# Kernel optimization log

Hardware: AMD Instinct MI355X
Metric: run time of the kernel (lower is better)

Reference implementation:

```python
import jax, jax.numpy as jnp
import numpy as np

ORIENTATIONS = 9
CELL = (8, 8)
BLOCK = (3, 3)
EPS = 1e-5  # skimage L2 block-norm epsilon


def _hog_features(x):
    # transform_sqrt=True (gamma compression)
    img = jnp.sqrt(x)
    H, W = img.shape
    # skimage _hog_channel_gradient: central differences, zero at borders
    g_row = jnp.zeros_like(img).at[1:-1, :].set(img[2:, :] - img[:-2, :])
    g_col = jnp.zeros_like(img).at[:, 1:-1].set(img[:, 2:] - img[:, :-2])
    mag = jnp.hypot(g_row, g_col)
    # orientation in degrees, folded to [0, 180)
    ori = jnp.rad2deg(jnp.arctan2(g_row, g_col)) % 180.0

    cr, cc = CELL
    ncr, ncc = H // cr, W // cc
    mag_c = mag[: ncr * cr, : ncc * cc]
    ori_c = ori[: ncr * cr, : ncc * cc]
    unit = 180.0 / ORIENTATIONS

    # hard binning (skimage uses no interpolation); small fixed loop over bins
    hists = []
    for b in range(ORIENTATIONS):
        sel = (ori_c >= b * unit) & (ori_c < (b + 1) * unit)
        m = jnp.where(sel, mag_c, 0.0)
        # per-cell mean of selected magnitudes: [ncr, ncc]
        cell = m.reshape(ncr, cr, ncc, cc).mean(axis=(1, 3))
        hists.append(cell)
    hist = jnp.stack(hists, axis=-1)  # [ncr, ncc, orientations]

    br_n, bc_n = BLOCK
    nbr, nbc = ncr - br_n + 1, ncc - bc_n + 1
    # overlapping blocks: [nbr, nbc, br_n, bc_n, orientations]
    blocks = jnp.stack(
        [jnp.stack([hist[i : i + nbr, j : j + nbc] for j in range(bc_n)], axis=2)
         for i in range(br_n)],
        axis=2,
    )
    # L2 block normalization: b / sqrt(sum(b^2) + eps^2)
    denom = jnp.sqrt(jnp.sum(blocks * blocks, axis=(2, 3, 4), keepdims=True) + EPS ** 2)
    normalized = blocks / denom
    return normalized.reshape(-1)  # feature_vector=True


def setup_inputs() -> dict:
    key = jax.random.key(0)
    x = jax.random.uniform(key, (4096, 4096), dtype=jnp.float32)
    return {"x": x}


def reference(x):
    return _hog_features(x)
```

## Files before the change

kernel.cpp:

```cpp
#include <hip/hip_runtime.h>
#include <math.h>

#define H 4096
#define W 4096
#define NC 512
#define NB 510
#define ORI 9
#define NCELLS (NC * NC)
#define NOUT (NB * NB * 81)

__device__ __forceinline__ float fdlibm_atanf(float x) {
#pragma clang fp contract(off)
    const float one = 1.0f;
    const float aT0  = (float) 3.33333333333329318027e-01;
    const float aT1  = (float)-1.99999999998764832476e-01;
    const float aT2  = (float) 1.42857142725034663711e-01;
    const float aT3  = (float)-1.11111104054623557880e-01;
    const float aT4  = (float) 9.09088713343650656196e-02;
    const float aT5  = (float)-7.69187620504482999495e-02;
    const float aT6  = (float) 6.66107313738753120669e-02;
    const float aT7  = (float)-5.83357013379057348645e-02;
    const float aT8  = (float) 4.97687799461593236017e-02;
    const float aT9  = (float)-3.65315727442169155270e-02;
    const float aT10 = (float) 1.62858201153657823623e-02;
    const float athi[4] = {4.6364760399e-01f, 7.8539812565e-01f,
                           9.8279368877e-01f, 1.5707962513e+00f};
    const float atlo[4] = {5.0121582440e-09f, 3.7748947079e-08f,
                           3.4473217170e-08f, 7.5497894159e-08f};
    int hx = __float_as_int(x);
    int ix = hx & 0x7fffffff;
    int id;
    if (ix >= 0x4c800000) {
        if (ix > 0x7f800000) return x + x;
        float r = athi[3] + atlo[3];
        return (hx > 0) ? r : -r;
    }
    if (ix < 0x3ee00000) {
        if (ix < 0x31000000) return x;
        id = -1;
    } else {
        x = fabsf(x);
        if (ix < 0x3f980000) {
            if (ix < 0x3f300000) { id = 0; x = (2.0f * x - one) / (2.0f + x); }
            else                 { id = 1; x = (x - one) / (x + one); }
        } else {
            if (ix < 0x401c0000) { id = 2; x = (x - 1.5f) / (one + 1.5f * x); }
            else                 { id = 3; x = -1.0f / x; }
        }
    }
    float z = x * x;
    float w = z * z;
    float s1 = z * (aT0 + w * (aT2 + w * (aT4 + w * (aT6 + w * (aT8 + w * aT10)))));
    float s2 = w * (aT1 + w * (aT3 + w * (aT5 + w * (aT7 + w * aT9))));
    if (id < 0) return x - x * (s1 + s2);
    z = athi[id] - ((x * (s1 + s2) - atlo[id]) - x);
    return (hx < 0) ? -z : z;
}

__device__ __forceinline__ float fdlibm_atan2f(float y, float x) {
#pragma clang fp contract(off)
    const float tiny   = 1.0e-30f;
    const float pi     = 3.1415927410e+00f;
    const float pi_lo  = -8.7422776573e-08f;
    const float pi_o_2 = 1.5707963705e+00f;
    int hx = __float_as_int(x), ix = hx & 0x7fffffff;
    int hy = __float_as_int(y), iy = hy & 0x7fffffff;
    if (hx == 0x3f800000) return fdlibm_atanf(y);
    int m = ((hy >> 31) & 1) | ((hx >> 30) & 2);
    if (iy == 0) {
        switch (m) {
            case 0: case 1: return y;
            case 2: return pi + tiny;
            default: return -pi - tiny;
        }
    }
    if (ix == 0) return (hy < 0) ? -pi_o_2 - tiny : pi_o_2 + tiny;
    int k = (iy - ix) >> 23;
    float z;
    if (k > 26) { z = pi_o_2 + 0.5f * pi_lo; m &= 1; }
    else if (k < -26 && hx < 0) z = 0.0f;
    else z = fdlibm_atanf(fabsf(y / x));
    switch (m) {
        case 0: return z;
        case 1: return -z;
        case 2: return pi - (z - pi_lo);
        default: return (z - pi_lo) - pi;
    }
}

__device__ __forceinline__ int slow_bin_px(const float* __restrict__ x,
                                           int grow, int gc,
                                           bool row_ok, bool col_ok) {
#pragma clang fp contract(off)
    float gy = 0.0f, gx = 0.0f;
    if (row_ok)
        gy = sqrtf(x[(grow + 1) * W + gc]) - sqrtf(x[(grow - 1) * W + gc]);
    if (col_ok)
        gx = sqrtf(x[grow * W + gc + 1]) - sqrtf(x[grow * W + gc - 1]);
    float ang = fdlibm_atan2f(gy, gx);
    const float RAD2DEG = (float)(180.0 / 3.14159265358979323846264338328);
    float deg = ang * RAD2DEG;
    float m = fmodf(deg, 180.0f);
    if (m < 0.0f) m += 180.0f;
    int bin = (int)(m / 20.0f);
    if (bin < 9 && m >= (float)((bin + 1) * 20)) bin++;
    else if (bin > 0 && m < (float)(bin * 20)) bin--;
    return bin;
}

#define T20 ((float) 0.36397023426620236135)
#define T40 ((float) 0.83909963117728001176)
#define T60 ((float) 1.73205080756887729353)
#define T80 ((float) 5.67128181961771110517)

__global__ __launch_bounds__(256, 4) void hog_hist(const float* __restrict__ x,
                                                   float* __restrict__ hist,
                                                   float* __restrict__ q) {
    int t = threadIdx.x;
    int w = t >> 6, lane = t & 63;
    int wid = blockIdx.x * 4 + w;
    int crow = wid >> 6;
    int strip = wid & 63;
    int gc = (strip << 6) + lane;

    int r0 = (crow << 3) - 1;
    int rtop = (r0 < 0) ? 0 : r0;
    int rbot = (r0 + 9 > H - 1) ? (H - 1) : (r0 + 9);
    int gcl = (gc == 0) ? 0 : gc - 1;
    int gcr = (gc == W - 1) ? (W - 1) : gc + 1;

    float s[10], sl[8], sr[8];
    s[0] = x[rtop * W + gc];
#pragma unroll
    for (int k = 1; k < 9; ++k) s[k] = x[(r0 + k) * W + gc];
    s[9] = x[rbot * W + gc];
#pragma unroll
    for (int j = 0; j < 8; ++j) {
        int grow = (crow << 3) + j;
        sl[j] = x[grow * W + gcl];
        sr[j] = x[grow * W + gcr];
    }
#pragma unroll
    for (int k = 0; k < 10; ++k) s[k] = __builtin_amdgcn_sqrtf(s[k]);
#pragma unroll
    for (int j = 0; j < 8; ++j) {
        sl[j] = __builtin_amdgcn_sqrtf(sl[j]);
        sr[j] = __builtin_amdgcn_sqrtf(sr[j]);
    }

    bool col_ok = (gc >= 1) && (gc <= W - 2);
    float acc[9];
#pragma unroll
    for (int b = 0; b < 9; ++b) acc[b] = 0.0f;
    unsigned gbits = 0;

#pragma unroll
    for (int j = 0; j < 8; ++j) {
        int grow = (crow << 3) + j;
        bool row_ok = (grow >= 1) && (grow <= H - 2);
        float gy = row_ok ? (s[j + 2] - s[j]) : 0.0f;
        float gx = col_ok ? (sr[j] - sl[j]) : 0.0f;

        float a = fabsf(gy), b = fabsf(gx);
        float d1 = fmaf(b, -T20, a);
        float d2 = fmaf(b, -T40, a);
        float d3 = fmaf(b, -T60, a);
        float d4 = fmaf(b, -T80, a);
        int cnt = (d1 > 0.0f) + (d2 > 0.0f) + (d3 > 0.0f) + (d4 > 0.0f);
        bool opp = ((__float_as_int(gy) ^ __float_as_int(gx)) < 0);
        int bin = opp ? 8 - cnt : cnt;

        float cm = fminf(fminf(fabsf(d1), fabsf(d2)),
                         fminf(fminf(fabsf(d3), fabsf(d4)), a));
        bool guard = cm < fmaf(1e-5f, a + b, 4e-6f);
        if (guard) { gbits |= (1u << j); bin = 15; }

        float mag = __builtin_amdgcn_sqrtf(fmaf(gy, gy, gx * gx));
#pragma unroll
        for (int bb = 0; bb < 9; ++bb) acc[bb] += (bin == bb) ? mag : 0.0f;
    }

    if (__any(gbits != 0)) {
#pragma unroll
        for (int j = 0; j < 8; ++j) {
            if ((gbits >> j) & 1u) {
                int grow = (crow << 3) + j;
                bool row_ok = (grow >= 1) && (grow <= H - 2);
                int bin = slow_bin_px(x, grow, gc, row_ok, col_ok);
                float gy = row_ok ? (s[j + 2] - s[j]) : 0.0f;
                float gx = col_ok ? (sr[j] - sl[j]) : 0.0f;
                float mag = __builtin_amdgcn_sqrtf(fmaf(gy, gy, gx * gx));
#pragma unroll
                for (int bb = 0; bb < 9; ++bb) acc[bb] += (bin == bb) ? mag : 0.0f;
            }
        }
    }

#pragma unroll
    for (int st = 1; st <= 4; st <<= 1) {
#pragma unroll
        for (int b = 0; b < 9; ++b) acc[b] += __shfl_xor(acc[b], st, 64);
    }

    int cell = lane >> 3;
    int k = lane & 7;
    int cbase = crow * (NC * ORI) + strip * 72 + cell * 9;
    float hv = acc[0];
#pragma unroll
    for (int b = 1; b < 8; ++b) hv = (k == b) ? acc[b] : hv;
    hist[cbase + k] = hv * (1.0f / 64.0f);
    if (k == 0) {
        hist[cbase + 8] = acc[8] * (1.0f / 64.0f);
        float qq = 0.0f;
#pragma unroll
        for (int b = 0; b < 9; ++b) {
            float h = acc[b] * (1.0f / 64.0f);
            qq = fmaf(h, h, qq);
        }
        q[crow * NC + strip * 8 + cell] = qq;
    }
}

__global__ __launch_bounds__(256) void hog_inv(const float* __restrict__ q,
                                               float* __restrict__ inv) {
    int t = blockIdx.x * 256 + threadIdx.x;
    if (t >= NB * NB) return;
    int i = t / NB;
    int j = t - i * NB;
    float ssq = 0.0f;
#pragma unroll
    for (int bi = 0; bi < 3; ++bi)
#pragma unroll
        for (int bj = 0; bj < 3; ++bj)
            ssq += q[(i + bi) * NC + (j + bj)];
    inv[t] = 1.0f / sqrtf(ssq + 1e-10f);
}

__global__ __launch_bounds__(256) void hog_norm(const float* __restrict__ hist,
                                                const float* __restrict__ inv,
                                                float* __restrict__ out, int n) {
    int k = blockIdx.x * 256 + threadIdx.x;
    if (k >= n) return;
    int pidx = k / 81;
    int e = k - pidx * 81;
    int i = pidx / NB;
    int j = pidx - i * NB;
    int bi = e / 27;
    int r = e - bi * 27;
    int bj = r / 9;
    int o = r - bj * 9;
    out[k] = hist[((i + bi) * NC + (j + bj)) * ORI + o] * inv[pidx];
}

extern "C" void kernel_launch(void* const* d_in, const int* in_sizes, int n_in,
                              void* d_out, int out_size, void* d_ws, size_t ws_size,
                              hipStream_t stream) {
    const float* x = (const float*)d_in[0];
    float* out = (float*)d_out;
    float* hist = (float*)d_ws;
    float* inv  = hist + NCELLS * ORI;
    float* q = out + (NOUT - NCELLS);

    hog_hist<<<(NC * 64) / 4, 256, 0, stream>>>(x, hist, q);
    hog_inv<<<(NB * NB + 255) / 256, 256, 0, stream>>>(q, inv);
    hog_norm<<<(out_size + 255) / 256, 256, 0, stream>>>(hist, inv, out, out_size);
}
```

Measured before the change: 76.10 us.

## Use threshold-count accumulators, DPP reductions, and vectorized float4 normalization stores

The histogram kernel no longer does a per-pixel 9-way select-accumulate. It keeps ten running sums: threshold counts split by sign quadrant. The nine bins are recovered afterwards by differencing. The cross-lane shuffle reduction within 8-lane groups becomes DPP row operations, which avoids LDS-based shuffles. The normalization kernel writes four outputs per thread as float4 stores. The differencing can introduce small floating-point rounding differences compared with direct accumulation, and the float4 path assumes out_size is divisible by 4.

```diff
diff --git a/kernel.cpp b/kernel.cpp
--- a/kernel.cpp
+++ b/kernel.cpp
@@ -113,6 +113,16 @@
 #define T60 ((float) 1.73205080756887729353)
 #define T80 ((float) 5.67128181961771110517)
 
+__device__ __forceinline__ float dpp_add8(float v) {
+    int t = __builtin_amdgcn_update_dpp(0, __float_as_int(v), 0xB1, 0xF, 0xF, true);
+    v += __int_as_float(t);
+    t = __builtin_amdgcn_update_dpp(0, __float_as_int(v), 0x4E, 0xF, 0xF, true);
+    v += __int_as_float(t);
+    t = __builtin_amdgcn_update_dpp(0, __float_as_int(v), 0x141, 0xF, 0xF, true);
+    v += __int_as_float(t);
+    return v;
+}
+
 __global__ __launch_bounds__(256, 4) void hog_hist(const float* __restrict__ x,
                                                    float* __restrict__ hist,
                                                    float* __restrict__ q) {
@@ -149,9 +159,8 @@
     }
 
     bool col_ok = (gc >= 1) && (gc <= W - 2);
-    float acc[9];
-#pragma unroll
-    for (int b = 0; b < 9; ++b) acc[b] = 0.0f;
+    float SA = 0.f, TA1 = 0.f, TA2 = 0.f, TA3 = 0.f, TA4 = 0.f;
+    float SB = 0.f, TB1 = 0.f, TB2 = 0.f, TB3 = 0.f, TB4 = 0.f;
     unsigned gbits = 0;
 
 #pragma unroll
@@ -166,19 +175,33 @@
         float d2 = fmaf(b, -T40, a);
         float d3 = fmaf(b, -T60, a);
         float d4 = fmaf(b, -T80, a);
-        int cnt = (d1 > 0.0f) + (d2 > 0.0f) + (d3 > 0.0f) + (d4 > 0.0f);
-        bool opp = ((__float_as_int(gy) ^ __float_as_int(gx)) < 0);
-        int bin = opp ? 8 - cnt : cnt;
 
         float cm = fminf(fminf(fabsf(d1), fabsf(d2)),
                          fminf(fminf(fabsf(d3), fabsf(d4)), a));
         bool guard = cm < fmaf(1e-5f, a + b, 4e-6f);
-        if (guard) { gbits |= (1u << j); bin = 15; }
-
+        if (guard) gbits |= (1u << j);
+
+        bool opp = ((__float_as_int(gy) ^ __float_as_int(gx)) < 0);
         float mag = __builtin_amdgcn_sqrtf(fmaf(gy, gy, gx * gx));
-#pragma unroll
-        for (int bb = 0; bb < 9; ++bb) acc[bb] += (bin == bb) ? mag : 0.0f;
-    }
+        float magA = (!opp && !guard) ? mag : 0.0f;
+        float magB = (opp && !guard) ? mag : 0.0f;
+
+        SA  += magA;
+        TA1 += (d1 > 0.0f) ? magA : 0.0f;
+        TA2 += (d2 > 0.0f) ? magA : 0.0f;
+        TA3 += (d3 > 0.0f) ? magA : 0.0f;
+        TA4 += (d4 > 0.0f) ? magA : 0.0f;
+        SB  += magB;
+        TB1 += (d1 > 0.0f) ? magB : 0.0f;
+        TB2 += (d2 > 0.0f) ? magB : 0.0f;
+        TB3 += (d3 > 0.0f) ? magB : 0.0f;
+        TB4 += (d4 > 0.0f) ? magB : 0.0f;
+    }
+
+    float bb[9];
+    bb[0] = SA - TA1;  bb[1] = TA1 - TA2;  bb[2] = TA2 - TA3;  bb[3] = TA3 - TA4;
+    bb[4] = TA4 + TB4;
+    bb[5] = TB3 - TB4; bb[6] = TB2 - TB3;  bb[7] = TB1 - TB2;  bb[8] = SB - TB1;
 
     if (__any(gbits != 0)) {
 #pragma unroll
@@ -191,30 +214,27 @@
                 float gx = col_ok ? (sr[j] - sl[j]) : 0.0f;
                 float mag = __builtin_amdgcn_sqrtf(fmaf(gy, gy, gx * gx));
 #pragma unroll
-                for (int bb = 0; bb < 9; ++bb) acc[bb] += (bin == bb) ? mag : 0.0f;
+                for (int b2 = 0; b2 < 9; ++b2) bb[b2] += (bin == b2) ? mag : 0.0f;
             }
         }
     }
 
 #pragma unroll
-    for (int st = 1; st <= 4; st <<= 1) {
-#pragma unroll
-        for (int b = 0; b < 9; ++b) acc[b] += __shfl_xor(acc[b], st, 64);
-    }
+    for (int b2 = 0; b2 < 9; ++b2) bb[b2] = dpp_add8(bb[b2]);
 
     int cell = lane >> 3;
     int k = lane & 7;
     int cbase = crow * (NC * ORI) + strip * 72 + cell * 9;
-    float hv = acc[0];
-#pragma unroll
-    for (int b = 1; b < 8; ++b) hv = (k == b) ? acc[b] : hv;
+    float hv = bb[0];
+#pragma unroll
+    for (int b2 = 1; b2 < 8; ++b2) hv = (k == b2) ? bb[b2] : hv;
     hist[cbase + k] = hv * (1.0f / 64.0f);
     if (k == 0) {
-        hist[cbase + 8] = acc[8] * (1.0f / 64.0f);
+        hist[cbase + 8] = bb[8] * (1.0f / 64.0f);
         float qq = 0.0f;
 #pragma unroll
-        for (int b = 0; b < 9; ++b) {
-            float h = acc[b] * (1.0f / 64.0f);
+        for (int b2 = 0; b2 < 9; ++b2) {
+            float h = bb[b2] * (1.0f / 64.0f);
             qq = fmaf(h, h, qq);
         }
         q[crow * NC + strip * 8 + cell] = qq;
@@ -236,20 +256,27 @@
     inv[t] = 1.0f / sqrtf(ssq + 1e-10f);
 }
 
-__global__ __launch_bounds__(256) void hog_norm(const float* __restrict__ hist,
-                                                const float* __restrict__ inv,
-                                                float* __restrict__ out, int n) {
-    int k = blockIdx.x * 256 + threadIdx.x;
-    if (k >= n) return;
-    int pidx = k / 81;
-    int e = k - pidx * 81;
-    int i = pidx / NB;
-    int j = pidx - i * NB;
-    int bi = e / 27;
-    int r = e - bi * 27;
-    int bj = r / 9;
-    int o = r - bj * 9;
-    out[k] = hist[((i + bi) * NC + (j + bj)) * ORI + o] * inv[pidx];
+__global__ __launch_bounds__(256) void hog_norm4(const float* __restrict__ hist,
+                                                 const float* __restrict__ inv,
+                                                 float4* __restrict__ out4, int n4) {
+    int v = blockIdx.x * 256 + threadIdx.x;
+    if (v >= n4) return;
+    int k0 = v * 4;
+    float r[4];
+#pragma unroll
+    for (int e = 0; e < 4; ++e) {
+        int k = k0 + e;
+        int pidx = k / 81;
+        int e81 = k - pidx * 81;
+        int i = pidx / NB;
+        int j = pidx - i * NB;
+        int bi = e81 / 27;
+        int rr = e81 - bi * 27;
+        int bj = rr / 9;
+        int o = rr - bj * 9;
+        r[e] = hist[((i + bi) * NC + (j + bj)) * ORI + o] * inv[pidx];
+    }
+    out4[v] = make_float4(r[0], r[1], r[2], r[3]);
 }
 
 extern "C" void kernel_launch(void* const* d_in, const int* in_sizes, int n_in,
@@ -263,5 +290,6 @@
 
     hog_hist<<<(NC * 64) / 4, 256, 0, stream>>>(x, hist, q);
     hog_inv<<<(NB * NB + 255) / 256, 256, 0, stream>>>(q, inv);
-    hog_norm<<<(out_size + 255) / 256, 256, 0, stream>>>(hist, inv, out, out_size);
-}
+    int n4 = out_size / 4;
+    hog_norm4<<<(n4 + 255) / 256, 256, 0, stream>>>(hist, inv, (float4*)out, n4);
+}
```

New measurement: 66.31 us. 1.15x faster.
